# Optimization experiments

Measured on AMD Instinct MI355X. Metric: run time of the kernel, lower is better.

The kernel has to match this reference:

```python
import jax, jax.numpy as jnp
import numpy as np

D_MODEL = 1024
HIDDEN = 4096
N_EXPERTS = 8
LB_COEF = 0.01
B, N = 2, 2048


def setup_inputs() -> dict:
    key = jax.random.key(0)
    k_x, k_g, k_w1, k_w2 = jax.random.split(key, 4)
    s = 0.02
    return {
        "x": jax.random.normal(k_x, (B, N, D_MODEL), dtype=jnp.float32),
        "gate_w": jax.random.normal(k_g, (N_EXPERTS, D_MODEL), dtype=jnp.float32) * s,
        "w1": jax.random.normal(k_w1, (N_EXPERTS, HIDDEN, D_MODEL), dtype=jnp.float32) * s,  # torch Linear weight [out,in]
        "b1": jnp.zeros((N_EXPERTS, HIDDEN), dtype=jnp.float32),
        "w2": jax.random.normal(k_w2, (N_EXPERTS, D_MODEL, HIDDEN), dtype=jnp.float32) * s,
        "b2": jnp.zeros((N_EXPERTS, D_MODEL), dtype=jnp.float32),
    }


def reference(x, gate_w, w1, b1, w2, b2):
    # gate logits: Linear(d_model, E, bias=False)
    logits = jnp.einsum('bnd,ed->bne', x, gate_w)
    probs = jax.nn.softmax(logits, axis=-1)            # router_prob
    gate_scores = jnp.max(probs, axis=-1)              # top-1 prob [B,N]
    sel = jnp.argmax(probs, axis=-1)                   # selected expert [B,N]

    # load-balance aux loss
    onehot = jax.nn.one_hot(sel, N_EXPERTS, dtype=x.dtype)
    f = onehot.mean(axis=(0, 1))                       # fraction of tokens per expert
    P = probs.mean(axis=(0, 1))                        # mean router prob per expert
    aux_loss = LB_COEF * N_EXPERTS * jnp.sum(f * P)

    # dispatch: loop over fixed small expert count (structurally distinct weights)
    out = jnp.zeros_like(x)
    for e in range(N_EXPERTS):
        h = jax.nn.gelu(jnp.einsum('bnd,hd->bnh', x, w1[e]) + b1[e], approximate=False)
        y = jnp.einsum('bnh,dh->bnd', h, w2[e]) + b2[e]
        out = out + jnp.where((sel == e)[..., None], gate_scores[..., None] * y, jnp.zeros((), x.dtype))
    return out, aux_loss
```

## Files before the change

### kernel.cpp

```cpp
#include <hip/hip_runtime.h>
#include <math.h>

#define T_TOK 4096
#define DM 1024
#define HID 4096
#define NEXP 8
#define MAXT 39

typedef unsigned short u16;
typedef __attribute__((ext_vector_type(8))) short short8;
typedef __attribute__((ext_vector_type(4))) float f32x4;

__device__ __forceinline__ u16 f2bf(float f){
  unsigned u = __float_as_uint(f);
  u += 0x7FFF + ((u >> 16) & 1);
  return (u16)(u >> 16);
}

#define GATE_OFF   0u
#define CNT_OFF    16384u
#define LIST_OFF   16512u
#define PROBS_OFF  147584u
#define XB_OFF     278656u
#define H_OFF      8667264u
#define W1B_OFF    42221696u
#define PART_OFF   W1B_OFF
#define W2B_OFF    109330560u

__device__ __forceinline__ void glds16(const void* g, void* l){
  __builtin_amdgcn_global_load_lds((const __attribute__((address_space(1))) void*)g,
                                   (__attribute__((address_space(3))) void*)l, 16, 0, 0);
}

__global__ void zero_cnt_kernel(int* cnt){
  if (threadIdx.x < NEXP) cnt[threadIdx.x] = 0;
}

__global__ __launch_bounds__(256) void cvt_kernel(const float* __restrict__ src,
                                                  u16* __restrict__ dst){
  size_t i = (size_t)blockIdx.x * 256 + threadIdx.x;
  const float4* s = (const float4*)src + i * 2;
  float4 a = s[0], b = s[1];
  uint4 p;
  p.x = (unsigned)f2bf(a.x) | ((unsigned)f2bf(a.y) << 16);
  p.y = (unsigned)f2bf(a.z) | ((unsigned)f2bf(a.w) << 16);
  p.z = (unsigned)f2bf(b.x) | ((unsigned)f2bf(b.y) << 16);
  p.w = (unsigned)f2bf(b.z) | ((unsigned)f2bf(b.w) << 16);
  ((uint4*)dst)[i] = p;
}

__global__ __launch_bounds__(256) void gate_kernel(
    const float* __restrict__ x, const float* __restrict__ gw,
    float* __restrict__ gateo, int* __restrict__ cnt, int* __restrict__ list,
    float* __restrict__ probs, u16* __restrict__ xb)
{
  int tid = threadIdx.x;
  int lane = tid & 63;
  int w = tid >> 6;
  int t = blockIdx.x * 4 + w;

  const float4* x4 = (const float4*)(x + (size_t)t * DM);
  const float4* g4 = (const float4*)gw;

  float acc[8] = {0,0,0,0,0,0,0,0};
  #pragma unroll
  for (int i = 0; i < 4; i++){
    int p = i * 64 + lane;
    float4 xv = x4[p];
    ushort4 pk;
    pk.x = f2bf(xv.x); pk.y = f2bf(xv.y); pk.z = f2bf(xv.z); pk.w = f2bf(xv.w);
    *(ushort4*)&xb[(size_t)t * DM + (size_t)p * 4] = pk;
    #pragma unroll
    for (int e = 0; e < NEXP; e++){
      float4 gv = g4[e * 256 + p];
      acc[e] += xv.x * gv.x + xv.y * gv.y + xv.z * gv.z + xv.w * gv.w;
    }
  }
  #pragma unroll
  for (int e = 0; e < NEXP; e++){
    #pragma unroll
    for (int off = 32; off; off >>= 1)
      acc[e] += __shfl_xor(acc[e], off);
  }
  if (lane == 0){
    float mx = acc[0];
    #pragma unroll
    for (int e = 1; e < NEXP; e++) mx = fmaxf(mx, acc[e]);
    float p[8]; float s = 0.f;
    #pragma unroll
    for (int e = 0; e < NEXP; e++){ p[e] = expf(acc[e] - mx); s += p[e]; }
    float inv = 1.f / s;
    int be = 0; float bp = p[0];
    #pragma unroll
    for (int e = 1; e < NEXP; e++){ if (p[e] > bp){ bp = p[e]; be = e; } }
    #pragma unroll
    for (int e = 0; e < NEXP; e++) probs[(size_t)t * 8 + e] = p[e] * inv;
    gateo[t] = bp * inv;
    int pos = atomicAdd(&cnt[be], 1);
    list[be * T_TOK + pos] = t;
  }
}

__global__ __launch_bounds__(256) void aux_kernel(
    const float* __restrict__ probs, const int* __restrict__ cnt,
    float* __restrict__ aux_out)
{
  __shared__ float sm[256 * 8];
  int tid = threadIdx.x;
  float s[8] = {0,0,0,0,0,0,0,0};
  for (int i = 0; i < 16; i++){
    int t = i * 256 + tid;
    #pragma unroll
    for (int e = 0; e < 8; e++) s[e] += probs[(size_t)t * 8 + e];
  }
  #pragma unroll
  for (int e = 0; e < 8; e++) sm[tid * 8 + e] = s[e];
  __syncthreads();
  for (int st = 128; st; st >>= 1){
    if (tid < st){
      #pragma unroll
      for (int e = 0; e < 8; e++) sm[tid * 8 + e] += sm[(tid + st) * 8 + e];
    }
    __syncthreads();
  }
  if (tid == 0){
    float a = 0.f;
    #pragma unroll
    for (int e = 0; e < 8; e++){
      float f = (float)cnt[e] / (float)T_TOK;
      float P = sm[e] / (float)T_TOK;
      a += f * P;
    }
    aux_out[0] = 0.01f * (float)NEXP * a;
  }
}

template<int ASTR, int BSTR, int NTOT, int NT, int KS, bool PHASE2>
__global__ __launch_bounds__(256, 3) void ffn_gemm(
    const u16*  __restrict__ Aall,
    const u16*  __restrict__ Bb,
    const float* __restrict__ bias,
    const int*  __restrict__ cnt,
    const int*  __restrict__ list,
    u16*  __restrict__ hOut,
    float* __restrict__ pOut)
{
  int bid = blockIdx.x;
  int nt = bid % NT;
  int r1 = bid / NT;
  int t  = r1 % MAXT;
  int sk = r1 / MAXT;

  int e = -1, mt = 0, accT = 0;
  #pragma unroll
  for (int i = 0; i < NEXP; i++){
    int nti = (cnt[i] + 127) >> 7;
    if (e < 0 && t < accT + nti){ e = i; mt = t - accT; }
    accT += nti;
  }
  if (e < 0) return;
  int ne = cnt[e];
  int m0 = mt * 128;
  const int* lst = list + e * T_TOK;
  int n0 = nt * 128;
  int koff = sk * (KS * 64);

  __shared__ u16 As[8192];
  __shared__ u16 Bs[8192];

  int tid  = threadIdx.x;
  int lane = tid & 63;
  int w    = tid >> 6;
  int wm = w >> 1, wn = w & 1;
  int fr = lane & 15, fq = lane >> 4;

  const u16* aS[4]; const u16* bS[4]; int dst[4];
  #pragma unroll
  for (int i = 0; i < 4; i++){
    int seg = w * 4 + i;
    int r   = seg * 8 + (lane >> 3);
    int g   = (lane & 7) ^ (r & 7);
    int mrow = m0 + r; if (mrow > ne - 1) mrow = ne - 1;
    aS[i] = Aall + (size_t)lst[mrow] * ASTR + koff + g * 8;
    bS[i] = Bb + (size_t)e * NTOT * BSTR + (size_t)(n0 + r) * BSTR + koff + g * 8;
    dst[i] = seg * 512;
  }

  f32x4 acc[4][4];
  #pragma unroll
  for (int m = 0; m < 4; m++)
    #pragma unroll
    for (int n = 0; n < 4; n++)
      acc[m][n] = (f32x4){0.f, 0.f, 0.f, 0.f};

  for (int ks = 0; ks < KS; ++ks){
    if (ks) __syncthreads();
    size_t ko = (size_t)ks * 64;
    #pragma unroll
    for (int i = 0; i < 4; i++) glds16(aS[i] + ko, &As[dst[i]]);
    #pragma unroll
    for (int i = 0; i < 4; i++) glds16(bS[i] + ko, &Bs[dst[i]]);
    __syncthreads();
    #pragma unroll
    for (int kc = 0; kc < 2; kc++){
      short8 afr[4], bfr[4];
      #pragma unroll
      for (int m = 0; m < 4; m++){
        int row  = wm * 64 + m * 16 + fr;
        int slot = (kc * 4 + fq) ^ (row & 7);
        afr[m] = *(const short8*)&As[row * 64 + slot * 8];
      }
      #pragma unroll
      for (int n = 0; n < 4; n++){
        int row  = wn * 64 + n * 16 + fr;
        int slot = (kc * 4 + fq) ^ (row & 7);
        bfr[n] = *(const short8*)&Bs[row * 64 + slot * 8];
      }
      #pragma unroll
      for (int m = 0; m < 4; m++)
        #pragma unroll
        for (int n = 0; n < 4; n++)
          acc[m][n] = __builtin_amdgcn_mfma_f32_16x16x32_bf16(afr[m], bfr[n], acc[m][n], 0, 0, 0);
    }
  }

  #pragma unroll
  for (int n = 0; n < 4; n++){
    int col = n0 + wn * 64 + n * 16 + fr;
    float bv = bias[(size_t)e * NTOT + col];
    if (PHASE2 && sk != 0) bv = 0.f;
    #pragma unroll
    for (int m = 0; m < 4; m++){
      int rbase = m0 + wm * 64 + m * 16 + fq * 4;
      f32x4 v = acc[m][n];
      #pragma unroll
      for (int i = 0; i < 4; i++){
        int mrow = rbase + i;
        if (mrow < ne){
          int tok = lst[mrow];
          float val = v[i] + bv;
          if (PHASE2){
            pOut[((size_t)sk * T_TOK + tok) * DM + col] = val;
          } else {
            float gl = 0.5f * val * (1.0f + erff(val * 0.70710678118654752f));
            hOut[(size_t)tok * HID + col] = f2bf(gl);
          }
        }
      }
    }
  }
}

__global__ __launch_bounds__(256) void reduce_kernel(
    const float* __restrict__ part, const float* __restrict__ gate,
    float* __restrict__ out)
{
  size_t i = (size_t)blockIdx.x * 256 + threadIdx.x;
  constexpr size_t S = (size_t)T_TOK * DM / 4;
  const float4* p = (const float4*)part;
  float4 a = p[i], b = p[i + S], c = p[i + 2 * S], d = p[i + 3 * S];
  float g = gate[i >> 8];
  float4 o;
  o.x = (a.x + b.x + c.x + d.x) * g;
  o.y = (a.y + b.y + c.y + d.y) * g;
  o.z = (a.z + b.z + c.z + d.z) * g;
  o.w = (a.w + b.w + c.w + d.w) * g;
  ((float4*)out)[i] = o;
}

extern "C" void kernel_launch(void* const* d_in, const int* in_sizes, int n_in,
                              void* d_out, int out_size, void* d_ws, size_t ws_size,
                              hipStream_t stream) {
  const float* x   = (const float*)d_in[0];
  const float* gw  = (const float*)d_in[1];
  const float* w1  = (const float*)d_in[2];
  const float* b1  = (const float*)d_in[3];
  const float* w2  = (const float*)d_in[4];
  const float* b2  = (const float*)d_in[5];

  char* ws = (char*)d_ws;
  float* gateo = (float*)(ws + GATE_OFF);
  int*   cnt   = (int*)  (ws + CNT_OFF);
  int*   list  = (int*)  (ws + LIST_OFF);
  float* probs = (float*)(ws + PROBS_OFF);
  u16*   xb    = (u16*)  (ws + XB_OFF);
  u16*   h     = (u16*)  (ws + H_OFF);
  u16*   w1b   = (u16*)  (ws + W1B_OFF);
  float* part  = (float*)(ws + PART_OFF);
  u16*   w2b   = (u16*)  (ws + W2B_OFF);

  float* out = (float*)d_out;
  float* aux = out + (size_t)T_TOK * DM;

  hipLaunchKernelGGL(zero_cnt_kernel, dim3(1), dim3(64), 0, stream, cnt);
  hipLaunchKernelGGL(gate_kernel, dim3(T_TOK / 4), dim3(256), 0, stream,
                     x, gw, gateo, cnt, list, probs, xb);
  hipLaunchKernelGGL(aux_kernel, dim3(1), dim3(256), 0, stream, probs, cnt, aux);
  hipLaunchKernelGGL(cvt_kernel, dim3(16384), dim3(256), 0, stream, w1, w1b);
  hipLaunchKernelGGL(cvt_kernel, dim3(16384), dim3(256), 0, stream, w2, w2b);

  hipLaunchKernelGGL((ffn_gemm<DM, DM, HID, 32, 16, false>),
                     dim3(MAXT * 32), dim3(256), 0, stream,
                     xb, w1b, b1, cnt, list, h, (float*)nullptr);
  hipLaunchKernelGGL((ffn_gemm<HID, HID, DM, 8, 16, true>),
                     dim3(4 * MAXT * 8), dim3(256), 0, stream,
                     h, w2b, b2, cnt, list, (u16*)nullptr, part);
  hipLaunchKernelGGL(reduce_kernel, dim3(T_TOK * DM / 4 / 256), dim3(256), 0, stream,
                     part, gateo, out);
}
```

Before: 311.3 us.

## Fuse fp32-to-bf16 weight conversion into GEMM tile loading

Removes the standalone conversion kernels for w1 and w2 and instead loads fp32 weight tiles into registers inside the FFN GEMMs, converting to bf16 before storing to LDS, with a one-step register prefetch of the next K slice. This avoids writing and rereading full bf16 weight copies. In exchange, each weight tile is fetched as fp32 by every M-tile block, doubling bytes per reuse, and the B path loses the async global-to-LDS loads while raising register pressure.

Result: faster. 302.1 us (-3.0%).

```diff
diff --git a/kernel.cpp b/kernel.cpp
--- a/kernel.cpp
+++ b/kernel.cpp
@@ -23,9 +23,7 @@
 #define PROBS_OFF  147584u
 #define XB_OFF     278656u
 #define H_OFF      8667264u
-#define W1B_OFF    42221696u
-#define PART_OFF   W1B_OFF
-#define W2B_OFF    109330560u
+#define PART_OFF   42221696u
 
 __device__ __forceinline__ void glds16(const void* g, void* l){
   __builtin_amdgcn_global_load_lds((const __attribute__((address_space(1))) void*)g,
@@ -34,19 +32,6 @@
 
 __global__ void zero_cnt_kernel(int* cnt){
   if (threadIdx.x < NEXP) cnt[threadIdx.x] = 0;
-}
-
-__global__ __launch_bounds__(256) void cvt_kernel(const float* __restrict__ src,
-                                                  u16* __restrict__ dst){
-  size_t i = (size_t)blockIdx.x * 256 + threadIdx.x;
-  const float4* s = (const float4*)src + i * 2;
-  float4 a = s[0], b = s[1];
-  uint4 p;
-  p.x = (unsigned)f2bf(a.x) | ((unsigned)f2bf(a.y) << 16);
-  p.y = (unsigned)f2bf(a.z) | ((unsigned)f2bf(a.w) << 16);
-  p.z = (unsigned)f2bf(b.x) | ((unsigned)f2bf(b.y) << 16);
-  p.w = (unsigned)f2bf(b.z) | ((unsigned)f2bf(b.w) << 16);
-  ((uint4*)dst)[i] = p;
 }
 
 __global__ __launch_bounds__(256) void gate_kernel(
@@ -138,7 +123,7 @@
 template<int ASTR, int BSTR, int NTOT, int NT, int KS, bool PHASE2>
 __global__ __launch_bounds__(256, 3) void ffn_gemm(
     const u16*  __restrict__ Aall,
-    const u16*  __restrict__ Bb,
+    const float* __restrict__ Bf,
     const float* __restrict__ bias,
     const int*  __restrict__ cnt,
     const int*  __restrict__ list,
@@ -174,7 +159,7 @@
   int wm = w >> 1, wn = w & 1;
   int fr = lane & 15, fq = lane >> 4;
 
-  const u16* aS[4]; const u16* bS[4]; int dst[4];
+  const u16* aS[4]; int aDst[4];
   #pragma unroll
   for (int i = 0; i < 4; i++){
     int seg = w * 4 + i;
@@ -182,8 +167,17 @@
     int g   = (lane & 7) ^ (r & 7);
     int mrow = m0 + r; if (mrow > ne - 1) mrow = ne - 1;
     aS[i] = Aall + (size_t)lst[mrow] * ASTR + koff + g * 8;
-    bS[i] = Bb + (size_t)e * NTOT * BSTR + (size_t)(n0 + r) * BSTR + koff + g * 8;
-    dst[i] = seg * 512;
+    aDst[i] = seg * 512;
+  }
+
+  const float* bS[4]; int bDst[4];
+  #pragma unroll
+  for (int i = 0; i < 4; i++){
+    int c = i * 256 + tid;
+    int r = c >> 3, sl = c & 7;
+    int g = sl ^ (r & 7);
+    bS[i] = Bf + ((size_t)e * NTOT + n0 + r) * BSTR + koff + g * 8;
+    bDst[i] = r * 64 + sl * 8;
   }
 
   f32x4 acc[4][4];
@@ -192,14 +186,35 @@
     #pragma unroll
     for (int n = 0; n < 4; n++)
       acc[m][n] = (f32x4){0.f, 0.f, 0.f, 0.f};
+
+  float4 br0[4], br1[4];
+  #pragma unroll
+  for (int i = 0; i < 4; i++){
+    const float4* s = (const float4*)bS[i];
+    br0[i] = s[0]; br1[i] = s[1];
+  }
 
   for (int ks = 0; ks < KS; ++ks){
     if (ks) __syncthreads();
     size_t ko = (size_t)ks * 64;
     #pragma unroll
-    for (int i = 0; i < 4; i++) glds16(aS[i] + ko, &As[dst[i]]);
-    #pragma unroll
-    for (int i = 0; i < 4; i++) glds16(bS[i] + ko, &Bs[dst[i]]);
+    for (int i = 0; i < 4; i++) glds16(aS[i] + ko, &As[aDst[i]]);
+    #pragma unroll
+    for (int i = 0; i < 4; i++){
+      uint4 pk;
+      pk.x = (unsigned)f2bf(br0[i].x) | ((unsigned)f2bf(br0[i].y) << 16);
+      pk.y = (unsigned)f2bf(br0[i].z) | ((unsigned)f2bf(br0[i].w) << 16);
+      pk.z = (unsigned)f2bf(br1[i].x) | ((unsigned)f2bf(br1[i].y) << 16);
+      pk.w = (unsigned)f2bf(br1[i].z) | ((unsigned)f2bf(br1[i].w) << 16);
+      *(uint4*)&Bs[bDst[i]] = pk;
+    }
+    if (ks + 1 < KS){
+      #pragma unroll
+      for (int i = 0; i < 4; i++){
+        const float4* s = (const float4*)(bS[i] + (ks + 1) * 64);
+        br0[i] = s[0]; br1[i] = s[1];
+      }
+    }
     __syncthreads();
     #pragma unroll
     for (int kc = 0; kc < 2; kc++){
@@ -285,9 +300,7 @@
   float* probs = (float*)(ws + PROBS_OFF);
   u16*   xb    = (u16*)  (ws + XB_OFF);
   u16*   h     = (u16*)  (ws + H_OFF);
-  u16*   w1b   = (u16*)  (ws + W1B_OFF);
   float* part  = (float*)(ws + PART_OFF);
-  u16*   w2b   = (u16*)  (ws + W2B_OFF);
 
   float* out = (float*)d_out;
   float* aux = out + (size_t)T_TOK * DM;
@@ -296,15 +309,13 @@
   hipLaunchKernelGGL(gate_kernel, dim3(T_TOK / 4), dim3(256), 0, stream,
                      x, gw, gateo, cnt, list, probs, xb);
   hipLaunchKernelGGL(aux_kernel, dim3(1), dim3(256), 0, stream, probs, cnt, aux);
-  hipLaunchKernelGGL(cvt_kernel, dim3(16384), dim3(256), 0, stream, w1, w1b);
-  hipLaunchKernelGGL(cvt_kernel, dim3(16384), dim3(256), 0, stream, w2, w2b);
 
   hipLaunchKernelGGL((ffn_gemm<DM, DM, HID, 32, 16, false>),
                      dim3(MAXT * 32), dim3(256), 0, stream,
-                     xb, w1b, b1, cnt, list, h, (float*)nullptr);
+                     xb, w1, b1, cnt, list, h, (float*)nullptr);
   hipLaunchKernelGGL((ffn_gemm<HID, HID, DM, 8, 16, true>),
                      dim3(4 * MAXT * 8), dim3(256), 0, stream,
-                     h, w2b, b2, cnt, list, (u16*)nullptr, part);
+                     h, w2, b2, cnt, list, (u16*)nullptr, part);
   hipLaunchKernelGGL(reduce_kernel, dim3(T_TOK * DM / 4 / 256), dim3(256), 0, stream,
                      part, gateo, out);
 }
```
